# Performance work log

Hardware: AMD Instinct MI355X
Metric: run time of the kernel (lower is better)

The kernel has to match this reference:

```python
import jax, jax.numpy as jnp
import numpy as np

B, S, E, D = 4, 4096, 512, 64

def setup_inputs() -> dict:
    key = jax.random.key(0)
    kx, kq, kk, kv = jax.random.split(key, 4)
    # xavier_normal std = sqrt(2/(E+D))
    std = float(np.sqrt(2.0 / (E + D)))
    return {
        "x": jax.random.normal(kx, (B, S, E), dtype=jnp.float32),
        "WQ": jax.random.normal(kq, (E, D), dtype=jnp.float32) * std,
        "WK": jax.random.normal(kk, (E, D), dtype=jnp.float32) * std,
        "WV": jax.random.normal(kv, (E, D), dtype=jnp.float32) * std,
    }

def reference(x, WQ, WK, WV):
    # Single-head causal attention; NOTE: scale uses embedding_size (E), as in source.
    Q = x @ WQ  # [B,S,D]
    K = x @ WK
    V = x @ WV
    scale = 1.0 / jnp.sqrt(jnp.float32(E))
    scores = jnp.einsum("bqd,bkd->bqk", Q, K) * scale  # [B,S,S]
    s = scores.shape[1]
    causal = jnp.tril(jnp.ones((s, s), dtype=bool))  # True = keep
    scores = jnp.where(causal[None, :, :], scores, -jnp.inf)
    attn = jax.nn.softmax(scores, axis=2)
    return jnp.einsum("bqk,bkd->bqd", attn, V)
```

## Files before the change

kernel.cpp:

```cpp
#include <hip/hip_runtime.h>
#include <hip/hip_bf16.h>

namespace {
constexpr int B = 4, S = 4096, E = 512, D = 64;
constexpr int NS = 8;
constexpr float SCALE_LOG2E = 0.04419417382415922f * 1.4426950408889634f;

typedef __bf16 bf16x8 __attribute__((ext_vector_type(8)));
typedef float floatx4 __attribute__((ext_vector_type(4)));
}

__global__ __launch_bounds__(256) void prep_wt(
    const float* __restrict__ WQ, const float* __restrict__ WK,
    const float* __restrict__ WV, __bf16* __restrict__ Wt)
{
    __shared__ __bf16 tile[64][72];
    const int t = threadIdx.x;
    const int mat = blockIdx.x >> 3;
    const int k0  = (blockIdx.x & 7) * 64;
    const float* W = (mat == 0) ? WQ : (mat == 1) ? WK : WV;
    #pragma unroll
    for (int i = 0; i < 16; ++i) {
        const int k = (t >> 6) + i * 4;
        tile[t & 63][k] = (__bf16)W[(k0 + k) * 64 + (t & 63)];
    }
    __syncthreads();
    #pragma unroll
    for (int i = 0; i < 2; ++i) {
        const int u = t + 256 * i;
        const int n = u >> 3, kseg = (u & 7) * 8;
        *(bf16x8*)(Wt + (mat * 64 + n) * 512 + k0 + kseg) =
            *(const bf16x8*)&tile[n][kseg];
    }
}

__global__ __launch_bounds__(256) void qkv_mfma(
    const float* __restrict__ x, const __bf16* __restrict__ Wt,
    __bf16* __restrict__ Qb, __bf16* __restrict__ Kb, __bf16* __restrict__ Vt)
{
    __shared__ __bf16 xs[32][72];
    __shared__ __bf16 ws[192][72];
    __shared__ __bf16 vsh[64][40];

    const int t = threadIdx.x;
    const int wave = t >> 6, lane = t & 63, quad = lane >> 4, l16 = lane & 15;
    const long row0 = (long)blockIdx.x * 32;

    const int xrr = t >> 3, xcc = (t & 7) * 8;

    floatx4 acc[2][3];
    #pragma unroll
    for (int m = 0; m < 2; ++m)
        #pragma unroll
        for (int n = 0; n < 3; ++n) acc[m][n] = (floatx4){0.f, 0.f, 0.f, 0.f};

    float4 xf0, xf1;
    bf16x8 wf[6];
    {
        const float* src = x + (row0 + xrr) * E + xcc;
        xf0 = *(const float4*)src;
        xf1 = *(const float4*)(src + 4);
        #pragma unroll
        for (int i = 0; i < 6; ++i) {
            const int c = t + 256 * i;
            wf[i] = *(const bf16x8*)(Wt + (c >> 3) * 512 + (c & 7) * 8);
        }
    }

    for (int kc = 0; kc < 8; ++kc) {
        __syncthreads();
        {
            bf16x8 v;
            v[0] = (__bf16)xf0.x; v[1] = (__bf16)xf0.y;
            v[2] = (__bf16)xf0.z; v[3] = (__bf16)xf0.w;
            v[4] = (__bf16)xf1.x; v[5] = (__bf16)xf1.y;
            v[6] = (__bf16)xf1.z; v[7] = (__bf16)xf1.w;
            *(bf16x8*)&xs[xrr][xcc] = v;
            #pragma unroll
            for (int i = 0; i < 6; ++i) {
                const int c = t + 256 * i;
                *(bf16x8*)&ws[c >> 3][(c & 7) * 8] = wf[i];
            }
        }
        __syncthreads();

        if (kc < 7) {
            const float* src = x + (row0 + xrr) * E + (kc + 1) * 64 + xcc;
            xf0 = *(const float4*)src;
            xf1 = *(const float4*)(src + 4);
            #pragma unroll
            for (int i = 0; i < 6; ++i) {
                const int c = t + 256 * i;
                wf[i] = *(const bf16x8*)(Wt + (c >> 3) * 512 + (kc + 1) * 64 + (c & 7) * 8);
            }
        }

        bf16x8 aa[2][2];
        #pragma unroll
        for (int m = 0; m < 2; ++m)
            #pragma unroll
            for (int ch = 0; ch < 2; ++ch)
                aa[m][ch] = *(const bf16x8*)&xs[m * 16 + l16][ch * 32 + quad * 8];
        #pragma unroll
        for (int ns = 0; ns < 3; ++ns) {
            #pragma unroll
            for (int ch = 0; ch < 2; ++ch) {
                bf16x8 bb = *(const bf16x8*)&ws[wave * 48 + ns * 16 + l16][ch * 32 + quad * 8];
                #pragma unroll
                for (int m = 0; m < 2; ++m)
                    acc[m][ns] = __builtin_amdgcn_mfma_f32_16x16x32_bf16(aa[m][ch], bb, acc[m][ns], 0, 0, 0);
            }
        }
    }

    const long bb_ = row0 >> 12;
    const int s0 = (int)(row0 & 4095);
    #pragma unroll
    for (int ns = 0; ns < 3; ++ns) {
        const int g = wave * 3 + ns;
        const int mat = g >> 2;
        const int col = (g & 3) * 16 + l16;
        #pragma unroll
        for (int m = 0; m < 2; ++m) {
            if (mat < 2) {
                __bf16* Out = (mat == 0) ? Qb : Kb;
                #pragma unroll
                for (int r = 0; r < 4; ++r)
                    Out[(row0 + m * 16 + quad * 4 + r) * 64 + col] = (__bf16)acc[m][ns][r];
            } else {
                __bf16 p[4];
                #pragma unroll
                for (int r = 0; r < 4; ++r) p[r] = (__bf16)acc[m][ns][r];
                *(unsigned long long*)&vsh[col][m * 16 + quad * 4] = *(unsigned long long*)p;
            }
        }
    }
    __syncthreads();
    {
        const int d = t >> 2, seg = (t & 3) * 8;
        bf16x8 v = *(const bf16x8*)&vsh[d][seg];
        *(bf16x8*)(Vt + (bb_ * 64 + d) * 4096 + s0 + seg) = v;
    }
}

__global__ __launch_bounds__(256) void attn_kernel(
    const __bf16* __restrict__ Qg, const __bf16* __restrict__ Kg,
    const __bf16* __restrict__ Vt, __bf16* __restrict__ Opart,
    float* __restrict__ Lpart)
{
    __shared__ __bf16 Ks[64][72];
    __shared__ __bf16 Vts[64][72];
    __shared__ __bf16 Ps[4][16][72];

    const int qt = 63 - blockIdx.x;
    const int c  = blockIdx.y;
    const int b  = blockIdx.z;
    const int q0 = qt * 64;
    const int t  = threadIdx.x;
    const int wave = t >> 6, lane = t & 63, quad = lane >> 4, l16 = lane & 15;

    const int nkt    = qt + 1;
    const int cs     = (nkt + NS - 1) / NS;
    const int kstart = c * cs;
    const int kend   = min(kstart + cs, nkt);

    const __bf16* qrow = Qg + ((long)(b * S + q0 + wave * 16 + l16)) * D;
    bf16x8 aq[2];
    aq[0] = *(const bf16x8*)(qrow + quad * 8);
    aq[1] = *(const bf16x8*)(qrow + 32 + quad * 8);

    bf16x8 ones;
    #pragma unroll
    for (int j = 0; j < 8; ++j) ones[j] = (__bf16)1.0f;

    floatx4 o[4];
    #pragma unroll
    for (int i = 0; i < 4; ++i) o[i] = (floatx4){0.f, 0.f, 0.f, 0.f};
    floatx4 lsum = (floatx4){0.f, 0.f, 0.f, 0.f};

    const int srow = t >> 2;
    const int sseg = (t & 3) * 16;

    bf16x8 kf0, kf1, vf0, vf1;
    if (kstart < kend) {
        const __bf16* ks = Kg + ((long)(b * S + kstart * 64 + srow)) * D + sseg;
        kf0 = *(const bf16x8*)ks;
        kf1 = *(const bf16x8*)(ks + 8);
        const __bf16* vs = Vt + ((long)(b * 64 + srow)) * 4096 + kstart * 64 + sseg;
        vf0 = *(const bf16x8*)vs;
        vf1 = *(const bf16x8*)(vs + 8);
    }

    for (int ktg = kstart; ktg < kend; ++ktg) {
        const int kbase = ktg * 64;
        __syncthreads();
        *(bf16x8*)&Ks[srow][sseg]      = kf0;
        *(bf16x8*)&Ks[srow][sseg + 8]  = kf1;
        *(bf16x8*)&Vts[srow][sseg]     = vf0;
        *(bf16x8*)&Vts[srow][sseg + 8] = vf1;
        __syncthreads();

        if (ktg + 1 < kend) {
            const __bf16* ks = Kg + ((long)(b * S + kbase + 64 + srow)) * D + sseg;
            kf0 = *(const bf16x8*)ks;
            kf1 = *(const bf16x8*)(ks + 8);
            const __bf16* vs = Vt + ((long)(b * 64 + srow)) * 4096 + kbase + 64 + sseg;
            vf0 = *(const bf16x8*)vs;
            vf1 = *(const bf16x8*)(vs + 8);
        }

        floatx4 sf[4];
        #pragma unroll
        for (int ns = 0; ns < 4; ++ns) {
            floatx4 cacc = (floatx4){0.f, 0.f, 0.f, 0.f};
            #pragma unroll
            for (int ch = 0; ch < 2; ++ch) {
                bf16x8 bk = *(const bf16x8*)&Ks[ns * 16 + l16][ch * 32 + quad * 8];
                cacc = __builtin_amdgcn_mfma_f32_16x16x32_bf16(aq[ch], bk, cacc, 0, 0, 0);
            }
            sf[ns] = cacc;
        }

        if (ktg == nkt - 1) {
            #pragma unroll
            for (int ns = 0; ns < 4; ++ns) {
                const int key = kbase + ns * 16 + l16;
                #pragma unroll
                for (int r = 0; r < 4; ++r) {
                    const int qr = q0 + wave * 16 + quad * 4 + r;
                    if (key > qr) sf[ns][r] = -1e30f;
                }
            }
        }

        #pragma unroll
        for (int ns = 0; ns < 4; ++ns)
            #pragma unroll
            for (int r = 0; r < 4; ++r) {
                float p = __builtin_amdgcn_exp2f(sf[ns][r] * SCALE_LOG2E);
                Ps[wave][quad * 4 + r][ns * 16 + l16] = (__bf16)p;
            }

        bf16x8 ap[2];
        ap[0] = *(const bf16x8*)&Ps[wave][l16][quad * 8];
        ap[1] = *(const bf16x8*)&Ps[wave][l16][32 + quad * 8];

        lsum = __builtin_amdgcn_mfma_f32_16x16x32_bf16(ap[0], ones, lsum, 0, 0, 0);
        lsum = __builtin_amdgcn_mfma_f32_16x16x32_bf16(ap[1], ones, lsum, 0, 0, 0);

        #pragma unroll
        for (int dsb = 0; dsb < 4; ++dsb) {
            floatx4 cacc = o[dsb];
            #pragma unroll
            for (int ch = 0; ch < 2; ++ch) {
                bf16x8 bv = *(const bf16x8*)&Vts[dsb * 16 + l16][ch * 32 + quad * 8];
                cacc = __builtin_amdgcn_mfma_f32_16x16x32_bf16(ap[ch], bv, cacc, 0, 0, 0);
            }
            o[dsb] = cacc;
        }
    }

    const long rbase = (long)c * (B * S) + (long)b * S + q0 + wave * 16;
    #pragma unroll
    for (int dsb = 0; dsb < 4; ++dsb)
        #pragma unroll
        for (int r = 0; r < 4; ++r)
            Opart[(rbase + quad * 4 + r) * 64 + dsb * 16 + l16] = (__bf16)o[dsb][r];
    if (l16 == 0) {
        #pragma unroll
        for (int r = 0; r < 4; ++r)
            Lpart[rbase + quad * 4 + r] = lsum[r];
    }
}

__global__ __launch_bounds__(256) void combine_kernel(
    const __bf16* __restrict__ Opart, const float* __restrict__ Lpart,
    float* __restrict__ Og)
{
    const int idx = blockIdx.x * 256 + threadIdx.x;
    const int row = idx >> 3, seg = (idx & 7) * 8;
    float acc[8] = {0, 0, 0, 0, 0, 0, 0, 0};
    float l = 0.f;
    #pragma unroll
    for (int c = 0; c < NS; ++c) {
        bf16x8 ov = *(const bf16x8*)(Opart + ((long)c * (B * S) + row) * 64 + seg);
        l += Lpart[(long)c * (B * S) + row];
        #pragma unroll
        for (int j = 0; j < 8; ++j) acc[j] += (float)ov[j];
    }
    const float invl = 1.f / l;
    float* dst = Og + (long)row * 64 + seg;
    float4 o0 = {acc[0] * invl, acc[1] * invl, acc[2] * invl, acc[3] * invl};
    float4 o1 = {acc[4] * invl, acc[5] * invl, acc[6] * invl, acc[7] * invl};
    *(float4*)dst = o0;
    *(float4*)(dst + 4) = o1;
}

extern "C" void kernel_launch(void* const* d_in, const int* in_sizes, int n_in,
                              void* d_out, int out_size, void* d_ws, size_t ws_size,
                              hipStream_t stream)
{
    const float* x  = (const float*)d_in[0];
    const float* WQ = (const float*)d_in[1];
    const float* WK = (const float*)d_in[2];
    const float* WV = (const float*)d_in[3];
    float* out = (float*)d_out;

    __bf16* Qb = (__bf16*)d_ws;
    __bf16* Kb = Qb + (size_t)B * S * D;
    __bf16* Vt = Kb + (size_t)B * S * D;
    __bf16* Wt = Vt + (size_t)B * S * D;
    __bf16* Opart = Wt + (size_t)3 * E * D;
    float*  Lpart = (float*)(Opart + (size_t)NS * B * S * D);

    prep_wt<<<dim3(24), 256, 0, stream>>>(WQ, WK, WV, Wt);
    qkv_mfma<<<dim3((B * S) / 32), 256, 0, stream>>>(x, Wt, Qb, Kb, Vt);
    attn_kernel<<<dim3(S / 64, NS, B), 256, 0, stream>>>(Qb, Kb, Vt, Opart, Lpart);
    combine_kernel<<<dim3((B * S * 8) / 256), 256, 0, stream>>>(Opart, Lpart, out);
}
```

Baseline: 120.1 us.

## Use fixed-size key chunks with triangular grid mapping; load W fragments directly from global

The attention kernel now splits each query tile's causal key range into fixed chunks of 8 key tiles instead of 8 equal variable-size splits. A compact triangular block index, decoded with a small loop, launches only the blocks that have work, giving 288 evenly sized blocks per batch. The combine kernel sums only the partial results that exist for each row. Separately, the QKV projection kernel drops the shared-memory staging of weights and loads each wave's MFMA B fragments straight from global/L2 into registers. That saves LDS traffic and stores but issues more scattered global loads.

```diff
diff --git a/kernel.cpp b/kernel.cpp
--- a/kernel.cpp
+++ b/kernel.cpp
@@ -3,7 +3,7 @@
 
 namespace {
 constexpr int B = 4, S = 4096, E = 512, D = 64;
-constexpr int NS = 8;
+constexpr int CHUNK = 8;
 constexpr float SCALE_LOG2E = 0.04419417382415922f * 1.4426950408889634f;
 
 typedef __bf16 bf16x8 __attribute__((ext_vector_type(8)));
@@ -39,14 +39,14 @@
     __bf16* __restrict__ Qb, __bf16* __restrict__ Kb, __bf16* __restrict__ Vt)
 {
     __shared__ __bf16 xs[32][72];
-    __shared__ __bf16 ws[192][72];
     __shared__ __bf16 vsh[64][40];
 
     const int t = threadIdx.x;
     const int wave = t >> 6, lane = t & 63, quad = lane >> 4, l16 = lane & 15;
     const long row0 = (long)blockIdx.x * 32;
-
     const int xrr = t >> 3, xcc = (t & 7) * 8;
+
+    const __bf16* wbase = Wt + (wave * 48 + l16) * 512 + quad * 8;
 
     floatx4 acc[2][3];
     #pragma unroll
@@ -61,12 +61,13 @@
         xf0 = *(const float4*)src;
         xf1 = *(const float4*)(src + 4);
         #pragma unroll
-        for (int i = 0; i < 6; ++i) {
-            const int c = t + 256 * i;
-            wf[i] = *(const bf16x8*)(Wt + (c >> 3) * 512 + (c & 7) * 8);
-        }
-    }
-
+        for (int ns = 0; ns < 3; ++ns)
+            #pragma unroll
+            for (int ch = 0; ch < 2; ++ch)
+                wf[ns * 2 + ch] = *(const bf16x8*)(wbase + ns * 16 * 512 + ch * 32);
+    }
+
+    #pragma unroll
     for (int kc = 0; kc < 8; ++kc) {
         __syncthreads();
         {
@@ -76,23 +77,23 @@
             v[4] = (__bf16)xf1.x; v[5] = (__bf16)xf1.y;
             v[6] = (__bf16)xf1.z; v[7] = (__bf16)xf1.w;
             *(bf16x8*)&xs[xrr][xcc] = v;
-            #pragma unroll
-            for (int i = 0; i < 6; ++i) {
-                const int c = t + 256 * i;
-                *(bf16x8*)&ws[c >> 3][(c & 7) * 8] = wf[i];
-            }
         }
         __syncthreads();
+
+        bf16x8 wcur[6];
+        #pragma unroll
+        for (int i = 0; i < 6; ++i) wcur[i] = wf[i];
 
         if (kc < 7) {
             const float* src = x + (row0 + xrr) * E + (kc + 1) * 64 + xcc;
             xf0 = *(const float4*)src;
             xf1 = *(const float4*)(src + 4);
             #pragma unroll
-            for (int i = 0; i < 6; ++i) {
-                const int c = t + 256 * i;
-                wf[i] = *(const bf16x8*)(Wt + (c >> 3) * 512 + (kc + 1) * 64 + (c & 7) * 8);
-            }
+            for (int ns = 0; ns < 3; ++ns)
+                #pragma unroll
+                for (int ch = 0; ch < 2; ++ch)
+                    wf[ns * 2 + ch] =
+                        *(const bf16x8*)(wbase + ns * 16 * 512 + (kc + 1) * 64 + ch * 32);
         }
 
         bf16x8 aa[2][2];
@@ -105,10 +106,10 @@
         for (int ns = 0; ns < 3; ++ns) {
             #pragma unroll
             for (int ch = 0; ch < 2; ++ch) {
-                bf16x8 bb = *(const bf16x8*)&ws[wave * 48 + ns * 16 + l16][ch * 32 + quad * 8];
                 #pragma unroll
                 for (int m = 0; m < 2; ++m)
-                    acc[m][ns] = __builtin_amdgcn_mfma_f32_16x16x32_bf16(aa[m][ch], bb, acc[m][ns], 0, 0, 0);
+                    acc[m][ns] = __builtin_amdgcn_mfma_f32_16x16x32_bf16(
+                        aa[m][ch], wcur[ns * 2 + ch], acc[m][ns], 0, 0, 0);
             }
         }
     }
@@ -152,17 +153,21 @@
     __shared__ __bf16 Vts[64][72];
     __shared__ __bf16 Ps[4][16][72];
 
-    const int qt = 63 - blockIdx.x;
-    const int c  = blockIdx.y;
-    const int b  = blockIdx.z;
+    int g = blockIdx.x;
+    int a = 0;
+    while (g >= 4 * (a + 1) * (a + 2)) ++a;
+    const int rem = g - 4 * a * (a + 1);
+    const int qt  = 8 * a + rem / (a + 1);
+    const int c   = rem % (a + 1);
+
+    const int b  = blockIdx.y;
     const int q0 = qt * 64;
     const int t  = threadIdx.x;
     const int wave = t >> 6, lane = t & 63, quad = lane >> 4, l16 = lane & 15;
 
     const int nkt    = qt + 1;
-    const int cs     = (nkt + NS - 1) / NS;
-    const int kstart = c * cs;
-    const int kend   = min(kstart + cs, nkt);
+    const int kstart = c * CHUNK;
+    const int kend   = min(kstart + CHUNK, nkt);
 
     const __bf16* qrow = Qg + ((long)(b * S + q0 + wave * 16 + l16)) * D;
     bf16x8 aq[2];
@@ -182,7 +187,7 @@
     const int sseg = (t & 3) * 16;
 
     bf16x8 kf0, kf1, vf0, vf1;
-    if (kstart < kend) {
+    {
         const __bf16* ks = Kg + ((long)(b * S + kstart * 64 + srow)) * D + sseg;
         kf0 = *(const bf16x8*)ks;
         kf1 = *(const bf16x8*)(ks + 8);
@@ -279,10 +284,11 @@
 {
     const int idx = blockIdx.x * 256 + threadIdx.x;
     const int row = idx >> 3, seg = (idx & 7) * 8;
+    const int qt = (row & (S - 1)) >> 6;
+    const int nc = (qt >> 3) + 1;
     float acc[8] = {0, 0, 0, 0, 0, 0, 0, 0};
     float l = 0.f;
-    #pragma unroll
-    for (int c = 0; c < NS; ++c) {
+    for (int c = 0; c < nc; ++c) {
         bf16x8 ov = *(const bf16x8*)(Opart + ((long)c * (B * S) + row) * 64 + seg);
         l += Lpart[(long)c * (B * S) + row];
         #pragma unroll
@@ -311,10 +317,10 @@
     __bf16* Vt = Kb + (size_t)B * S * D;
     __bf16* Wt = Vt + (size_t)B * S * D;
     __bf16* Opart = Wt + (size_t)3 * E * D;
-    float*  Lpart = (float*)(Opart + (size_t)NS * B * S * D);
+    float*  Lpart = (float*)(Opart + (size_t)8 * B * S * D);
 
     prep_wt<<<dim3(24), 256, 0, stream>>>(WQ, WK, WV, Wt);
     qkv_mfma<<<dim3((B * S) / 32), 256, 0, stream>>>(x, Wt, Qb, Kb, Vt);
-    attn_kernel<<<dim3(S / 64, NS, B), 256, 0, stream>>>(Qb, Kb, Vt, Opart, Lpart);
+    attn_kernel<<<dim3(288, B), 256, 0, stream>>>(Qb, Kb, Vt, Opart, Lpart);
     combine_kernel<<<dim3((B * S * 8) / 256), 256, 0, stream>>>(Opart, Lpart, out);
 }
```

Measured after the change: 120.3 us. About the same (+0.1%).
